# Performance work log

Measured on AMD Instinct MI355X. Metric: run time of the kernel, lower is better.

The kernel has to match this reference:

```python
import jax, jax.numpy as jnp
import numpy as np
import math

N, C, L, D = 8, 16, 1024, 7   # x: [N, in_heads=C, L, in_features=D]
H = 16                        # out_heads
SZ = C * D                    # 112 (in_sz == out_sz since in_heads == out_heads)

def setup_inputs() -> dict:
    key = jax.random.key(0)
    ks = jax.random.split(key, 7)
    s = 1.0 / math.sqrt(SZ)
    return {
        "x":  jax.random.normal(ks[0], (N, C, L, D), dtype=jnp.float32),
        "Wq": jax.random.normal(ks[1], (SZ, SZ), dtype=jnp.float32) * s,
        "bq": jax.random.normal(ks[2], (SZ,), dtype=jnp.float32) * s,
        "Wk": jax.random.normal(ks[3], (SZ, SZ), dtype=jnp.float32) * s,
        "bk": jax.random.normal(ks[4], (SZ,), dtype=jnp.float32) * s,
        "Wv": jax.random.normal(ks[5], (SZ, SZ), dtype=jnp.float32) * s,
        "bv": jax.random.normal(ks[6], (SZ,), dtype=jnp.float32) * s,
    }

def _split_heads(t):
    # [N, L, H*d] -> [N, H, L, d]
    n, l, _ = t.shape
    return t.reshape(n, l, H, -1).transpose(0, 2, 1, 3)

def reference(x, Wq, bq, Wk, bk, Wv, bv):
    n, c, l, d = x.shape
    # [N, C, L, D] -> [N, L, C*D]
    xf = x.transpose(0, 2, 1, 3).reshape(n, l, c * d)
    q = _split_heads(xf @ Wq.T + bq)   # [N, H, L, d]
    k = _split_heads(xf @ Wk.T + bk)
    v = _split_heads(xf @ Wv.T + bv)
    scores = jnp.einsum('bhqd,bhkd->bhqk', q, k)
    # NOTE: original scales by sqrt(scores.shape[-1]) == sqrt(L), not sqrt(head_dim)
    scores = scores / jnp.sqrt(jnp.asarray(l, scores.dtype))
    weights = jax.nn.softmax(scores.astype(jnp.float32), axis=-1).astype(scores.dtype)
    # dropout p=0.5 is identity in eval mode
    return jnp.einsum('bhqk,bhkd->bhqd', weights, v)
```

## Files before the change

### kernel.cpp

```cpp
#include <hip/hip_runtime.h>
#include <math.h>

#define NB 8
#define CH 16
#define LL 1024
#define DD 7
#define HH 16

typedef float    v2f  __attribute__((ext_vector_type(2)));
typedef float    v4f  __attribute__((ext_vector_type(4)));
typedef float    v16f __attribute__((ext_vector_type(16)));
typedef short    v8s  __attribute__((ext_vector_type(8)));
typedef unsigned v4u  __attribute__((ext_vector_type(4)));

#if __has_builtin(__builtin_amdgcn_exp2f)
#define EXP2F(x) __builtin_amdgcn_exp2f(x)
#else
#define EXP2F(x) exp2f(x)
#endif

__device__ inline unsigned bf16_rne(float f) {
    unsigned u = __builtin_bit_cast(unsigned, f);
    return (u + 0x7fffu + ((u >> 16) & 1u)) >> 16;
}
__device__ inline unsigned pack_trunc(float a, float b) {
    unsigned ua = __builtin_bit_cast(unsigned, a);
    unsigned ub = __builtin_bit_cast(unsigned, b);
    return (ua >> 16) | (ub & 0xffff0000u);
}

__global__ __launch_bounds__(256, 2) void qkv_proj(
    const float* __restrict__ x,
    const float* __restrict__ Wq, const float* __restrict__ bq,
    const float* __restrict__ Wk, const float* __restrict__ bk,
    const float* __restrict__ Wv, const float* __restrict__ bv,
    unsigned short* __restrict__ qkvb)
{
    __shared__ __align__(16) unsigned short Wb[112 * 136];
    __shared__ __align__(16) unsigned short xb[64 * 136];

    int bx  = blockIdx.x;
    int mat = bx / (NB * 16);
    int rem = bx % (NB * 16);
    int n   = rem / 16;
    int l0  = (rem % 16) * 64;

    const float* W = (mat == 0) ? Wq : (mat == 1) ? Wk : Wv;
    const float* b = (mat == 0) ? bq : (mat == 1) ? bk : bv;

    int tid = threadIdx.x;

    {
        const float4* Wsrc = (const float4*)W;
        for (int i4 = tid; i4 < 3136; i4 += 256) {
            int j  = i4 / 28;
            int ii = (i4 - j * 28) * 4;
            float4 w = Wsrc[i4];
            unsigned lo = bf16_rne(w.x) | (bf16_rne(w.y) << 16);
            unsigned hi = bf16_rne(w.z) | (bf16_rne(w.w) << 16);
            *(uint2*)&Wb[j * 136 + ii] = make_uint2(lo, hi);
        }
    }
    for (int idx = tid; idx < 64 * 112; idx += 256) {
        int c  = idx / 448;
        int r  = idx - c * 448;
        int l  = r / 7;
        int dd = r - l * 7;
        xb[l * 136 + c * 7 + dd] =
            (unsigned short)bf16_rne(x[((n * CH + c) * LL + l0 + l) * DD + dd]);
    }
    for (int idx = tid; idx < 64 * 16; idx += 256)
        xb[(idx >> 4) * 136 + 112 + (idx & 15)] = 0;
    for (int idx = tid; idx < 112 * 16; idx += 256)
        Wb[(idx >> 4) * 136 + 112 + (idx & 15)] = 0;

    {
        size_t base = ((size_t)(mat * NB + n) * HH) * (LL * 8);
        for (int idx = tid; idx < 1024; idx += 256) {
            int hh = idx >> 6, l = idx & 63;
            qkvb[base + (size_t)(hh * LL + l0 + l) * 8 + 7] = 0;
        }
    }
    __syncthreads();

    int wv = tid >> 6, lane = tid & 63, l15 = lane & 15, l4 = lane >> 4;

    const unsigned short* Arow = xb + (wv * 16 + l15) * 136 + l4 * 8;
    v8s af[4];
    #pragma unroll
    for (int k4 = 0; k4 < 4; ++k4) af[k4] = *(const v8s*)(Arow + k4 * 32);

    v4f acc[7];
    #pragma unroll
    for (int jt = 0; jt < 7; ++jt) acc[jt] = (v4f){0.f, 0.f, 0.f, 0.f};

    #pragma unroll
    for (int jt = 0; jt < 7; ++jt) {
        const unsigned short* Brow = Wb + (jt * 16 + l15) * 136 + l4 * 8;
        #pragma unroll
        for (int k4 = 0; k4 < 4; ++k4) {
            v8s bf = *(const v8s*)(Brow + k4 * 32);
            acc[jt] = __builtin_amdgcn_mfma_f32_16x16x32_bf16(af[k4], bf, acc[jt], 0, 0, 0);
        }
    }

    const float scale = (mat == 0) ? 0.0450842200277801f  : 1.0f;
    size_t mbase = ((size_t)(mat * NB + n) * HH) * (LL * 8);
    #pragma unroll
    for (int jt = 0; jt < 7; ++jt) {
        int j   = jt * 16 + l15;
        int hh  = j / 7;
        int dim = j - hh * 7;
        float bj = b[j];
        int lrow = l0 + wv * 16 + l4 * 4;
        size_t rb = mbase + (size_t)hh * (LL * 8) + (size_t)lrow * 8 + dim;
        #pragma unroll
        for (int r = 0; r < 4; ++r) {
            float val = (acc[jt][r] + bj) * scale;
            qkvb[rb + (size_t)r * 8] = (unsigned short)bf16_rne(val);
        }
    }
}

__global__ __launch_bounds__(256, 4) void attn(
    const unsigned short* __restrict__ qkvb, float* __restrict__ out)
{
    __shared__ __align__(16) unsigned short Kl[LL * 8];
    __shared__ __align__(16) unsigned short Vt[8 * 1048];

    int bx = blockIdx.x;
    int qt = bx & 7, h = (bx >> 3) & 15, n = bx >> 7;
    int tid  = threadIdx.x;
    int wave = tid >> 6, lane = tid & 63;
    int l31 = lane & 31, g5 = lane >> 5;

    const unsigned short* Qg = qkvb + (size_t)((0 * NB + n) * HH + h) * (LL * 8);
    const unsigned short* Kg = qkvb + (size_t)((1 * NB + n) * HH + h) * (LL * 8);
    const unsigned short* Vg = qkvb + (size_t)((2 * NB + n) * HH + h) * (LL * 8);

    {
        const uint4* Ks = (const uint4*)Kg;
        uint4* Kd = (uint4*)Kl;
        #pragma unroll
        for (int it = 0; it < 4; ++it) Kd[tid + it * 256] = Ks[tid + it * 256];
    }
    {
        const uint4* Vs = (const uint4*)Vg;
        uint4 r0 = Vs[4 * tid], r1 = Vs[4 * tid + 1];
        uint4 r2 = Vs[4 * tid + 2], r3 = Vs[4 * tid + 3];
        const unsigned* p0 = (const unsigned*)&r0;
        const unsigned* p1 = (const unsigned*)&r1;
        const unsigned* p2 = (const unsigned*)&r2;
        const unsigned* p3 = (const unsigned*)&r3;
        int col = ((tid >> 3) << 5) + ((tid & 1) << 3) + (((tid >> 1) & 1) << 2)
                + (((tid >> 2) & 1) << 4);
        #pragma unroll
        for (int d = 0; d < 7; ++d) {
            unsigned a0 = p0[d >> 1], a1 = p1[d >> 1], a2 = p2[d >> 1], a3 = p3[d >> 1];
            unsigned w0, w1;
            if (d & 1) { w0 = (a0 >> 16) | (a1 & 0xffff0000u); w1 = (a2 >> 16) | (a3 & 0xffff0000u); }
            else       { w0 = (a0 & 0xffffu) | (a1 << 16);     w1 = (a2 & 0xffffu) | (a3 << 16); }
            *(uint2*)&Vt[d * 1048 + col] = make_uint2(w0, w1);
        }
        *(uint2*)&Vt[7 * 1048 + col] = make_uint2(0x3f803f80u, 0x3f803f80u);
    }
    __syncthreads();

    int q = qt * 128 + wave * 32 + l31;
    v8s zero8 = {0, 0, 0, 0, 0, 0, 0, 0};
    v8s qf = (lane < 32) ? *(const v8s*)(Qg + (size_t)q * 8) : zero8;

    const unsigned short* Vrow = Vt + (l31 & 7) * 1048 + g5 * 8;
    v16f acc = {};

    v8s kf = (lane < 32) ? *(const v8s*)(Kl + l31 * 8) : zero8;

    #pragma unroll 4
    for (int c = 0; c < 32; ++c) {
        v16f s = __builtin_amdgcn_mfma_f32_32x32x16_bf16(kf, qf, (v16f){}, 0, 0, 0);
        if (c < 31)
            kf = (lane < 32) ? *(const v8s*)(Kl + ((c + 1) * 32 + l31) * 8) : zero8;
        v8s va1 = *(const v8s*)(Vrow + c * 32);
        v8s va2 = *(const v8s*)(Vrow + c * 32 + 16);

        unsigned pk[8];
        #pragma unroll
        for (int p = 0; p < 8; ++p)
            pk[p] = pack_trunc(EXP2F(s[2 * p]), EXP2F(s[2 * p + 1]));
        v8s pA = __builtin_bit_cast(v8s, (v4u){pk[0], pk[1], pk[2], pk[3]});
        v8s pB = __builtin_bit_cast(v8s, (v4u){pk[4], pk[5], pk[6], pk[7]});

        acc = __builtin_amdgcn_mfma_f32_32x32x16_bf16(va1, pA, acc, 0, 0, 0);
        acc = __builtin_amdgcn_mfma_f32_32x32x16_bf16(va2, pB, acc, 0, 0, 0);
    }

    float rs = __shfl(acc[3], 32 + l31, 64);
    float* base = out + (size_t)(n * HH + h) * LL * 7 + (size_t)q * 7;
    #pragma unroll
    for (int r = 0; r < 4; ++r) {
        int dim = 4 * g5 + r;
        if (dim < 7) base[dim] = acc[r] / rs;
    }
}

extern "C" void kernel_launch(void* const* d_in, const int* in_sizes, int n_in,
                              void* d_out, int out_size, void* d_ws, size_t ws_size,
                              hipStream_t stream) {
    const float* x  = (const float*)d_in[0];
    const float* Wq = (const float*)d_in[1];
    const float* bq = (const float*)d_in[2];
    const float* Wk = (const float*)d_in[3];
    const float* bk = (const float*)d_in[4];
    const float* Wv = (const float*)d_in[5];
    const float* bv = (const float*)d_in[6];
    unsigned short* qkvb = (unsigned short*)d_ws;
    float* o = (float*)d_out;

    qkv_proj<<<dim3(3 * NB * 16), dim3(256), 0, stream>>>(x, Wq, bq, Wk, bk, Wv, bv, qkvb);
    attn<<<dim3(NB * HH * 8), dim3(256), 0, stream>>>(qkvb, o);
}
```

Measured before the change: 101.6 us.

## Process two 32-query tiles per wave in attention to reuse K/V fragments

Each attention wave now handles 64 queries as two independent 32-query tiles that share every K and V fragment loaded from LDS. The grid is halved accordingly, so the per-block K load and V transpose into LDS is amortized over twice as many queries. This cuts LDS reads and block setup and gives more independent MFMA work to interleave. The costs are more registers per wave (launch bounds lowered to 2 blocks), only 512 blocks on a 256-CU part, and lower occupancy.

Result: no change. 100.6 us (-0.9%).

```diff
diff --git a/kernel.cpp b/kernel.cpp
--- a/kernel.cpp
+++ b/kernel.cpp
@@ -122,14 +122,14 @@
     }
 }
 
-__global__ __launch_bounds__(256, 4) void attn(
+__global__ __launch_bounds__(256, 2) void attn(
     const unsigned short* __restrict__ qkvb, float* __restrict__ out)
 {
     __shared__ __align__(16) unsigned short Kl[LL * 8];
     __shared__ __align__(16) unsigned short Vt[8 * 1048];
 
     int bx = blockIdx.x;
-    int qt = bx & 7, h = (bx >> 3) & 15, n = bx >> 7;
+    int qt = bx & 3, h = (bx >> 2) & 15, n = bx >> 6;
     int tid  = threadIdx.x;
     int wave = tid >> 6, lane = tid & 63;
     int l31 = lane & 31, g5 = lane >> 5;
@@ -166,40 +166,62 @@
     }
     __syncthreads();
 
-    int q = qt * 128 + wave * 32 + l31;
+    int q0 = qt * 256 + wave * 64 + l31;
     v8s zero8 = {0, 0, 0, 0, 0, 0, 0, 0};
-    v8s qf = (lane < 32) ? *(const v8s*)(Qg + (size_t)q * 8) : zero8;
+    v8s qfA = (lane < 32) ? *(const v8s*)(Qg + (size_t)q0 * 8)        : zero8;
+    v8s qfB = (lane < 32) ? *(const v8s*)(Qg + (size_t)(q0 + 32) * 8) : zero8;
 
     const unsigned short* Vrow = Vt + (l31 & 7) * 1048 + g5 * 8;
-    v16f acc = {};
+    v16f accA = {}, accB = {};
 
     v8s kf = (lane < 32) ? *(const v8s*)(Kl + l31 * 8) : zero8;
 
-    #pragma unroll 4
+    #pragma unroll 2
     for (int c = 0; c < 32; ++c) {
-        v16f s = __builtin_amdgcn_mfma_f32_32x32x16_bf16(kf, qf, (v16f){}, 0, 0, 0);
+        v16f sA = __builtin_amdgcn_mfma_f32_32x32x16_bf16(kf, qfA, (v16f){}, 0, 0, 0);
+        v16f sB = __builtin_amdgcn_mfma_f32_32x32x16_bf16(kf, qfB, (v16f){}, 0, 0, 0);
         if (c < 31)
             kf = (lane < 32) ? *(const v8s*)(Kl + ((c + 1) * 32 + l31) * 8) : zero8;
         v8s va1 = *(const v8s*)(Vrow + c * 32);
         v8s va2 = *(const v8s*)(Vrow + c * 32 + 16);
 
-        unsigned pk[8];
+        unsigned pkA[8], pkB[8];
         #pragma unroll
         for (int p = 0; p < 8; ++p)
-            pk[p] = pack_trunc(EXP2F(s[2 * p]), EXP2F(s[2 * p + 1]));
-        v8s pA = __builtin_bit_cast(v8s, (v4u){pk[0], pk[1], pk[2], pk[3]});
-        v8s pB = __builtin_bit_cast(v8s, (v4u){pk[4], pk[5], pk[6], pk[7]});
-
-        acc = __builtin_amdgcn_mfma_f32_32x32x16_bf16(va1, pA, acc, 0, 0, 0);
-        acc = __builtin_amdgcn_mfma_f32_32x32x16_bf16(va2, pB, acc, 0, 0, 0);
-    }
-
-    float rs = __shfl(acc[3], 32 + l31, 64);
-    float* base = out + (size_t)(n * HH + h) * LL * 7 + (size_t)q * 7;
-    #pragma unroll
-    for (int r = 0; r < 4; ++r) {
-        int dim = 4 * g5 + r;
-        if (dim < 7) base[dim] = acc[r] / rs;
+            pkA[p] = pack_trunc(EXP2F(sA[2 * p]), EXP2F(sA[2 * p + 1]));
+        #pragma unroll
+        for (int p = 0; p < 8; ++p)
+            pkB[p] = pack_trunc(EXP2F(sB[2 * p]), EXP2F(sB[2 * p + 1]));
+
+        v8s pA1 = __builtin_bit_cast(v8s, (v4u){pkA[0], pkA[1], pkA[2], pkA[3]});
+        v8s pA2 = __builtin_bit_cast(v8s, (v4u){pkA[4], pkA[5], pkA[6], pkA[7]});
+        v8s pB1 = __builtin_bit_cast(v8s, (v4u){pkB[0], pkB[1], pkB[2], pkB[3]});
+        v8s pB2 = __builtin_bit_cast(v8s, (v4u){pkB[4], pkB[5], pkB[6], pkB[7]});
+
+        accA = __builtin_amdgcn_mfma_f32_32x32x16_bf16(va1, pA1, accA, 0, 0, 0);
+        accA = __builtin_amdgcn_mfma_f32_32x32x16_bf16(va2, pA2, accA, 0, 0, 0);
+        accB = __builtin_amdgcn_mfma_f32_32x32x16_bf16(va1, pB1, accB, 0, 0, 0);
+        accB = __builtin_amdgcn_mfma_f32_32x32x16_bf16(va2, pB2, accB, 0, 0, 0);
+    }
+
+    size_t hb = (size_t)(n * HH + h) * LL * 7;
+    {
+        float rs = __shfl(accA[3], 32 + l31, 64);
+        float* base = out + hb + (size_t)q0 * 7;
+        #pragma unroll
+        for (int r = 0; r < 4; ++r) {
+            int dim = 4 * g5 + r;
+            if (dim < 7) base[dim] = accA[r] / rs;
+        }
+    }
+    {
+        float rs = __shfl(accB[3], 32 + l31, 64);
+        float* base = out + hb + (size_t)(q0 + 32) * 7;
+        #pragma unroll
+        for (int r = 0; r < 4; ++r) {
+            int dim = 4 * g5 + r;
+            if (dim < 7) base[dim] = accB[r] / rs;
+        }
     }
 }
 
@@ -217,5 +239,5 @@
     float* o = (float*)d_out;
 
     qkv_proj<<<dim3(3 * NB * 16), dim3(256), 0, stream>>>(x, Wq, bq, Wk, bk, Wv, bv, qkvb);
-    attn<<<dim3(NB * HH * 8), dim3(256), 0, stream>>>(qkvb, o);
-}
+    attn<<<dim3(NB * HH * 4), dim3(256), 0, stream>>>(qkvb, o);
+}
```

## Split attention key range across two wave groups with software-pipelined score MFMA

Applied to the files above, without the earlier changes.

Doubles the attention block to 512 threads. Each of four query groups now has two waves, and each wave handles half of the 1024 keys; the partial numerators and denominators are combined through shared memory before the final division. The score MFMA for the next chunk is issued one iteration early so it overlaps the exp/pack and PV MFMAs. Each wave also starts at a rotated chunk offset to spread LDS bank accesses. The aim is shorter per-wave serial loops and more latency hiding, at the cost of an extra barrier, a shared-memory reduction, and larger blocks that may limit occupancy.

Measured after the change: 103.9 us. 1.02x slower.

```diff
diff --git a/kernel.cpp b/kernel.cpp
--- a/kernel.cpp
+++ b/kernel.cpp
@@ -122,17 +122,20 @@
     }
 }
 
-__global__ __launch_bounds__(256, 4) void attn(
+__global__ __launch_bounds__(512, 4) void attn(
     const unsigned short* __restrict__ qkvb, float* __restrict__ out)
 {
     __shared__ __align__(16) unsigned short Kl[LL * 8];
     __shared__ __align__(16) unsigned short Vt[8 * 1048];
+    __shared__ __align__(16) float red[128 * 8];
 
     int bx = blockIdx.x;
     int qt = bx & 7, h = (bx >> 3) & 15, n = bx >> 7;
     int tid  = threadIdx.x;
     int wave = tid >> 6, lane = tid & 63;
     int l31 = lane & 31, g5 = lane >> 5;
+    int g  = wave & 3;
+    int kh = wave >> 2;
 
     const unsigned short* Qg = qkvb + (size_t)((0 * NB + n) * HH + h) * (LL * 8);
     const unsigned short* Kg = qkvb + (size_t)((1 * NB + n) * HH + h) * (LL * 8);
@@ -141,10 +144,10 @@
     {
         const uint4* Ks = (const uint4*)Kg;
         uint4* Kd = (uint4*)Kl;
-        #pragma unroll
-        for (int it = 0; it < 4; ++it) Kd[tid + it * 256] = Ks[tid + it * 256];
-    }
-    {
+        Kd[tid]       = Ks[tid];
+        Kd[tid + 512] = Ks[tid + 512];
+    }
+    if (tid < 256) {
         const uint4* Vs = (const uint4*)Vg;
         uint4 r0 = Vs[4 * tid], r1 = Vs[4 * tid + 1];
         uint4 r2 = Vs[4 * tid + 2], r3 = Vs[4 * tid + 3];
@@ -166,40 +169,63 @@
     }
     __syncthreads();
 
-    int q = qt * 128 + wave * 32 + l31;
+    int q0 = qt * 128 + g * 32 + l31;
     v8s zero8 = {0, 0, 0, 0, 0, 0, 0, 0};
-    v8s qf = (lane < 32) ? *(const v8s*)(Qg + (size_t)q * 8) : zero8;
+    v8s qf = (lane < 32) ? *(const v8s*)(Qg + (size_t)q0 * 8) : zero8;
 
     const unsigned short* Vrow = Vt + (l31 & 7) * 1048 + g5 * 8;
     v16f acc = {};
 
-    v8s kf = (lane < 32) ? *(const v8s*)(Kl + l31 * 8) : zero8;
+    int kbase = kh * 512;
+    int rot   = (wave << 1) & 15;
+
+    #define KOFF(c) ((kbase + (((c) + rot) & 15) * 32))
+
+    v8s kf = (lane < 32) ? *(const v8s*)(Kl + KOFF(0) * 8 + l31 * 8) : zero8;
+    v16f s_cur = __builtin_amdgcn_mfma_f32_32x32x16_bf16(kf, qf, (v16f){}, 0, 0, 0);
+    kf = (lane < 32) ? *(const v8s*)(Kl + KOFF(1) * 8 + l31 * 8) : zero8;
 
     #pragma unroll 4
-    for (int c = 0; c < 32; ++c) {
-        v16f s = __builtin_amdgcn_mfma_f32_32x32x16_bf16(kf, qf, (v16f){}, 0, 0, 0);
-        if (c < 31)
-            kf = (lane < 32) ? *(const v8s*)(Kl + ((c + 1) * 32 + l31) * 8) : zero8;
-        v8s va1 = *(const v8s*)(Vrow + c * 32);
-        v8s va2 = *(const v8s*)(Vrow + c * 32 + 16);
+    for (int c = 0; c < 16; ++c) {
+        v16f s_nxt = s_cur;
+        if (c < 15)
+            s_nxt = __builtin_amdgcn_mfma_f32_32x32x16_bf16(kf, qf, (v16f){}, 0, 0, 0);
+        if (c < 14)
+            kf = (lane < 32) ? *(const v8s*)(Kl + KOFF(c + 2) * 8 + l31 * 8) : zero8;
+
+        v8s va1 = *(const v8s*)(Vrow + KOFF(c));
+        v8s va2 = *(const v8s*)(Vrow + KOFF(c) + 16);
 
         unsigned pk[8];
         #pragma unroll
         for (int p = 0; p < 8; ++p)
-            pk[p] = pack_trunc(EXP2F(s[2 * p]), EXP2F(s[2 * p + 1]));
-        v8s pA = __builtin_bit_cast(v8s, (v4u){pk[0], pk[1], pk[2], pk[3]});
-        v8s pB = __builtin_bit_cast(v8s, (v4u){pk[4], pk[5], pk[6], pk[7]});
-
-        acc = __builtin_amdgcn_mfma_f32_32x32x16_bf16(va1, pA, acc, 0, 0, 0);
-        acc = __builtin_amdgcn_mfma_f32_32x32x16_bf16(va2, pB, acc, 0, 0, 0);
-    }
-
-    float rs = __shfl(acc[3], 32 + l31, 64);
-    float* base = out + (size_t)(n * HH + h) * LL * 7 + (size_t)q * 7;
-    #pragma unroll
-    for (int r = 0; r < 4; ++r) {
-        int dim = 4 * g5 + r;
-        if (dim < 7) base[dim] = acc[r] / rs;
+            pk[p] = pack_trunc(EXP2F(s_cur[2 * p]), EXP2F(s_cur[2 * p + 1]));
+        v8s p1 = __builtin_bit_cast(v8s, (v4u){pk[0], pk[1], pk[2], pk[3]});
+        v8s p2 = __builtin_bit_cast(v8s, (v4u){pk[4], pk[5], pk[6], pk[7]});
+
+        acc = __builtin_amdgcn_mfma_f32_32x32x16_bf16(va1, p1, acc, 0, 0, 0);
+        acc = __builtin_amdgcn_mfma_f32_32x32x16_bf16(va2, p2, acc, 0, 0, 0);
+
+        s_cur = s_nxt;
+    }
+    #undef KOFF
+
+    if (kh == 1) {
+        *(float4*)&red[(size_t)(g * 32 + l31) * 8 + 4 * g5] =
+            make_float4(acc[0], acc[1], acc[2], acc[3]);
+    }
+    __syncthreads();
+    if (kh == 0) {
+        float4 pa = *(const float4*)&red[(size_t)(g * 32 + l31) * 8 + 4 * g5];
+        acc[0] += pa.x; acc[1] += pa.y; acc[2] += pa.z; acc[3] += pa.w;
+
+        float rs = __shfl(acc[3], 32 + l31, 64);
+        float* base = out + (size_t)(n * HH + h) * LL * 7 + (size_t)q0 * 7;
+        #pragma unroll
+        for (int r = 0; r < 4; ++r) {
+            int dim = 4 * g5 + r;
+            if (dim < 7) base[dim] = acc[r] / rs;
+        }
     }
 }
 
@@ -217,5 +243,5 @@
     float* o = (float*)d_out;
 
     qkv_proj<<<dim3(3 * NB * 16), dim3(256), 0, stream>>>(x, Wq, bq, Wk, bk, Wv, bv, qkvb);
-    attn<<<dim3(NB * HH * 8), dim3(256), 0, stream>>>(qkvb, o);
-}
+    attn<<<dim3(NB * HH * 8), dim3(512), 0, stream>>>(qkvb, o);
+}
```
